# Performance work log

Measured on AMD Instinct MI355X. Metric: run time of the kernel, lower is better.

Reference implementation:

```python
import jax, jax.numpy as jnp
import numpy as np

N = 100000      # nodes
E = 1600000     # edges (avg degree 16)
IN = 128
OUT = 256


def setup_inputs() -> dict:
    key = jax.random.key(0)
    ks = jax.random.split(key, 8)
    x = jax.random.normal(ks[0], (N, IN), dtype=jnp.float32)
    edge_index = jax.random.randint(ks[1], (2, E), 0, N, dtype=jnp.int64)
    # GCNConv weights (glorot-ish scale) and biases
    W1 = jax.random.normal(ks[2], (IN, OUT), dtype=jnp.float32) / np.float32(np.sqrt(IN))
    b1 = jnp.zeros((OUT,), jnp.float32)
    W2 = jax.random.normal(ks[3], (OUT, OUT), dtype=jnp.float32) / np.float32(np.sqrt(OUT))
    b2 = jnp.zeros((OUT,), jnp.float32)
    # projection Linear(IN, OUT)
    Wp = jax.random.normal(ks[4], (IN, OUT), dtype=jnp.float32) / np.float32(np.sqrt(IN))
    bp = jax.random.normal(ks[5], (OUT,), dtype=jnp.float32) * 0.01
    return {"x": x, "edge_index": edge_index, "W1": W1, "b1": b1,
            "W2": W2, "b2": b2, "Wp": Wp, "bp": bp}


def _gcn_conv(x, W, b, src, dst, n):
    """PyG GCNConv: D^{-1/2}(A+I)D^{-1/2} X W + b. src/dst already include self-loops."""
    xw = x @ W                                              # [n, out]
    ones = jnp.ones(src.shape[0], dtype=xw.dtype)
    deg = jax.ops.segment_sum(ones, dst, num_segments=n)    # in-degree incl. self-loop
    dinv = jnp.where(deg > 0, jax.lax.rsqrt(deg), 0.0)
    norm = dinv[src] * dinv[dst]                            # [e]
    msgs = xw[src] * norm[:, None]                          # gather + scale
    out = jax.ops.segment_sum(msgs, dst, num_segments=n)    # scatter-add
    return out + b


def reference(x, edge_index, W1, b1, W2, b2, Wp, bp):
    n = x.shape[0]
    loop = jnp.arange(n, dtype=edge_index.dtype)            # self-loops
    src = jnp.concatenate([edge_index[0], loop])
    dst = jnp.concatenate([edge_index[1], loop])
    out = jax.nn.relu(_gcn_conv(x, W1, b1, src, dst, n))
    out = _gcn_conv(out, W2, b2, src, dst, n)
    identity = x @ Wp + bp                                  # projection (IN != OUT)
    return jax.nn.relu(out + identity)
```

## Files before the change

### kernel.cpp

```cpp
#include <hip/hip_runtime.h>

#define NODES 100000
#define EDGES 1600000
#define FIN   128
#define FOUT  256
#define NBUCK 196

typedef __bf16 bf16;
typedef __bf16 bf16x8 __attribute__((ext_vector_type(8)));
typedef __bf16 bf16x4 __attribute__((ext_vector_type(4)));
typedef __bf16 bf16x2 __attribute__((ext_vector_type(2)));
typedef float  f32x4  __attribute__((ext_vector_type(4)));

__global__ __launch_bounds__(256) void detect_kernel(const void* __restrict__ x,
                                                     const int* __restrict__ ei,
                                                     int* __restrict__ flags) {
    __shared__ int s_f32_evidence;
    __shared__ int s_odd_nonzero;
    int t = threadIdx.x;
    if (t == 0) { s_f32_evidence = 0; s_odd_nonzero = 0; }
    __syncthreads();
    const bf16* xb = (const bf16*)x;
    int local_f32 = 0;
    for (int i = t; i < 4096; i += 256) {
        float v = fabsf((float)xb[i]);
        if (!(v < 1e4f)) local_f32 = 1;
    }
    if (local_f32) atomicOr(&s_f32_evidence, 1);
    int local_odd = 0;
    for (int k = t; k < 1024; k += 256) {
        if (ei[2 * k + 1] != 0) local_odd = 1;
    }
    if (local_odd) atomicOr(&s_odd_nonzero, 1);
    __syncthreads();
    if (t == 0) {
        flags[0] = s_f32_evidence ? 0 : 1;
        flags[1] = s_odd_nonzero ? 0 : 1;
    }
}

__device__ __forceinline__ int edge_at(const int* __restrict__ ei, int which, int i,
                                       int is64) {
    if (is64) return ei[2 * (which * EDGES + i)];
    return ei[which * EDGES + i];
}

__global__ __launch_bounds__(512) void deg_count(const int* __restrict__ ei,
                                                 int* __restrict__ deg,
                                                 int* __restrict__ bhist,
                                                 const int* __restrict__ flags) {
    __shared__ int lh[256];
    int t = threadIdx.x;
    if (t < 256) lh[t] = 0;
    __syncthreads();
    int i = blockIdx.x * 512 + t;
    if (i < EDGES) {
        int is64 = flags[1];
        int s = edge_at(ei, 0, i, is64);
        int d = edge_at(ei, 1, i, is64);
        if (s >= 0 && s < NODES && d >= 0 && d < NODES) {
            atomicAdd(&deg[d], 1);
            atomicAdd(&lh[d >> 9], 1);
        }
    }
    __syncthreads();
    if (t < NBUCK && lh[t] > 0) atomicAdd(&bhist[t], lh[t]);
}

__global__ __launch_bounds__(256) void deg_to_dinv(const int* __restrict__ deg,
                                                   float* __restrict__ dinv, int n) {
    int i = blockIdx.x * 256 + threadIdx.x;
    if (i < n) dinv[i] = rsqrtf((float)deg[i] + 1.0f);
}

__global__ __launch_bounds__(1024) void scan1(const int* __restrict__ deg,
                                              int* __restrict__ col_ptr,
                                              int* __restrict__ blksum, int n) {
    __shared__ int sm[1024];
    int t = threadIdx.x;
    int i = blockIdx.x * 1024 + t;
    int v = (i < n) ? deg[i] : 0;
    sm[t] = v;
    __syncthreads();
    for (int off = 1; off < 1024; off <<= 1) {
        int u = (t >= off) ? sm[t - off] : 0;
        __syncthreads();
        sm[t] += u;
        __syncthreads();
    }
    if (i <= n) col_ptr[i] = sm[t] - v;
    if (t == 1023) blksum[blockIdx.x] = sm[t];
}

__global__ __launch_bounds__(128) void scan2(int* blk, int nblk) {
    __shared__ int sm[128];
    int t = threadIdx.x;
    int v = (t < nblk) ? blk[t] : 0;
    sm[t] = v;
    __syncthreads();
    for (int off = 1; off < 128; off <<= 1) {
        int u = (t >= off) ? sm[t - off] : 0;
        __syncthreads();
        sm[t] += u;
        __syncthreads();
    }
    if (t < nblk) blk[t] = sm[t] - v;
}

__global__ __launch_bounds__(256) void scan3(int* __restrict__ col_ptr,
                                             const int* __restrict__ blkoff, int n) {
    int i = blockIdx.x * 256 + threadIdx.x;
    if (i <= n) col_ptr[i] += blkoff[i >> 10];
}

__global__ __launch_bounds__(256) void bucket_scan(const int* __restrict__ bhist,
                                                   int* __restrict__ bbase,
                                                   int* __restrict__ bcur) {
    __shared__ int sm[256];
    int t = threadIdx.x;
    int v = (t < NBUCK) ? bhist[t] : 0;
    sm[t] = v;
    __syncthreads();
    for (int off = 1; off < 256; off <<= 1) {
        int u = (t >= off) ? sm[t - off] : 0;
        __syncthreads();
        sm[t] += u;
        __syncthreads();
    }
    if (t < NBUCK) {
        int ex = sm[t] - v;
        bbase[t] = ex;
        bcur[t]  = ex;
        if (t == NBUCK - 1) bbase[NBUCK] = sm[t];
    }
}

#define EPB 4096
__global__ __launch_bounds__(256) void partition_edges(const int* __restrict__ ei,
                                                       int* __restrict__ bcur,
                                                       uint2* __restrict__ pairs,
                                                       const int* __restrict__ flags) {
    __shared__ int lh[256], sc[256], lst[256], lcu[256], gb[256];
    __shared__ uint2 stage[EPB];
    int t = threadIdx.x;
    int base = blockIdx.x * EPB;
    int is64 = flags[1];

    lh[t] = 0;
    __syncthreads();

    int es[16], ed[16];
#pragma unroll
    for (int j = 0; j < 16; ++j) {
        int i = base + j * 256 + t;
        int s = -1, d = -1;
        if (i < EDGES) {
            s = edge_at(ei, 0, i, is64);
            d = edge_at(ei, 1, i, is64);
            if (s < 0 || s >= NODES || d < 0 || d >= NODES) d = -1;
        }
        es[j] = s; ed[j] = d;
        if (d >= 0) atomicAdd(&lh[d >> 9], 1);
    }
    __syncthreads();
    sc[t] = lh[t];
    __syncthreads();
    for (int off = 1; off < 256; off <<= 1) {
        int u = (t >= off) ? sc[t - off] : 0;
        __syncthreads();
        sc[t] += u;
        __syncthreads();
    }
    int start = sc[t] - lh[t];
    lst[t] = start;
    lcu[t] = start;
    __syncthreads();
#pragma unroll
    for (int j = 0; j < 16; ++j) {
        if (ed[j] >= 0) {
            int p = atomicAdd(&lcu[ed[j] >> 9], 1);
            stage[p] = make_uint2((unsigned)es[j], (unsigned)ed[j]);
        }
    }
    __syncthreads();
    if (t < NBUCK && lh[t] > 0) gb[t] = atomicAdd(&bcur[t], lh[t]);
    __syncthreads();
    int nval = sc[255];
    for (int slot = t; slot < nval; slot += 256) {
        uint2 e = stage[slot];
        int b = (int)(e.y >> 9);
        pairs[(size_t)gb[b] + (slot - lst[b])] = e;
    }
}

__global__ __launch_bounds__(512) void fine_fill(const uint2* __restrict__ pairs,
                                                 const int* __restrict__ bbase,
                                                 const int* __restrict__ col_ptr,
                                                 int* __restrict__ col_idx) {
    __shared__ int lcur[512];
    int b = blockIdx.x;
    int t = threadIdx.x;
    int node = (b << 9) + t;
    lcur[t] = (node < NODES) ? col_ptr[node] : 0;
    __syncthreads();
    int beg = bbase[b], end = bbase[b + 1];
    for (int i = beg + t; i < end; i += 512) {
        uint2 e = pairs[i];
        int pos = atomicAdd(&lcur[e.y & 511], 1);
        col_idx[pos] = (int)e.x;
    }
}

__global__ __launch_bounds__(256) void pack_all(const void* __restrict__ W1,
                                                const void* __restrict__ W2,
                                                const void* __restrict__ Wp,
                                                const void* __restrict__ b1,
                                                const void* __restrict__ b2,
                                                const void* __restrict__ bp,
                                                bf16* __restrict__ W1p, bf16* __restrict__ W2p,
                                                bf16* __restrict__ Wpp, bf16* __restrict__ b1b,
                                                bf16* __restrict__ b2b, bf16* __restrict__ bpb,
                                                const int* __restrict__ flags) {
    int fl = flags[0];
    int b = blockIdx.x;
    if (b < 512) {
        const void* W; bf16* Wo; int idx;
        if (b < 128)      { W = W1; Wo = W1p; idx = b * 256 + threadIdx.x; }
        else if (b < 384) { W = W2; Wo = W2p; idx = (b - 128) * 256 + threadIdx.x; }
        else              { W = Wp; Wo = Wpp; idx = (b - 384) * 256 + threadIdx.x; }
        int j    = idx & 7;
        int lane = (idx >> 3) & 63;
        int ct   = (idx >> 9) & 15;
        int kt   = idx >> 13;
        int k = kt * 32 + (lane >> 4) * 8 + j;
        int n = ct * 16 + (lane & 15);
        Wo[idx] = fl ? ((const bf16*)W)[k * 256 + n]
                     : (bf16)(((const float*)W)[k * 256 + n]);
    } else {
        const void* bb; bf16* bo;
        if (b == 512)      { bb = b1; bo = b1b; }
        else if (b == 513) { bb = b2; bo = b2b; }
        else               { bb = bp; bo = bpb; }
        int i = threadIdx.x;
        bo[i] = fl ? ((const bf16*)bb)[i] : (bf16)(((const float*)bb)[i]);
    }
}

__global__ __launch_bounds__(256) void gemm_proj(const void* __restrict__ Av,
                                                 const bf16* __restrict__ Wpk,
                                                 const float* __restrict__ dinv,
                                                 const bf16* __restrict__ bias,
                                                 void* __restrict__ outv,
                                                 bf16* __restrict__ projb,
                                                 int use_projb,
                                                 bf16* __restrict__ Xs,
                                                 const int* __restrict__ flags) {
    int a_f32 = (flags[0] == 0);
    int wave = threadIdx.x >> 6;
    int lane = threadIdx.x & 63;
    int row0 = blockIdx.x * 64;
    int lr = lane & 15;
    int lk = (lane >> 4) * 8;

    int arow[4];
    float di4[4];
#pragma unroll
    for (int rf = 0; rf < 4; ++rf) {
        int r = row0 + rf * 16 + lr;
        arow[rf] = r < NODES ? r : (NODES - 1);
        di4[rf] = dinv[arow[rf]];
    }

    f32x4 acc[4][4];
    f32x4 z = {0.f, 0.f, 0.f, 0.f};
#pragma unroll
    for (int i = 0; i < 4; ++i)
#pragma unroll
        for (int j = 0; j < 4; ++j) acc[i][j] = z;

    for (int kt = 0; kt < 4; ++kt) {
        bf16x8 af[4];
        if (!a_f32) {
            const bf16* Ab = (const bf16*)Av + kt * 32 + lk;
#pragma unroll
            for (int rf = 0; rf < 4; ++rf)
                af[rf] = *(const bf16x8*)(Ab + (size_t)arow[rf] * FIN);
        } else {
            const float* Af = (const float*)Av + kt * 32 + lk;
#pragma unroll
            for (int rf = 0; rf < 4; ++rf) {
                const float* p = Af + (size_t)arow[rf] * FIN;
                f32x4 lo = *(const f32x4*)p;
                f32x4 hi = *(const f32x4*)(p + 4);
                af[rf][0] = (bf16)lo[0]; af[rf][1] = (bf16)lo[1];
                af[rf][2] = (bf16)lo[2]; af[rf][3] = (bf16)lo[3];
                af[rf][4] = (bf16)hi[0]; af[rf][5] = (bf16)hi[1];
                af[rf][6] = (bf16)hi[2]; af[rf][7] = (bf16)hi[3];
            }
        }
#pragma unroll
        for (int rf = 0; rf < 4; ++rf) {
            bf16x8 xsv;
#pragma unroll
            for (int j = 0; j < 8; ++j) xsv[j] = (bf16)(di4[rf] * (float)af[rf][j]);
            *(bf16x8*)(Xs + (size_t)arow[rf] * FIN + kt * 32 + lk) = xsv;
        }
        const bf16* wb = Wpk + ((size_t)(kt * 16 + wave * 4) * 64 + lane) * 8;
        bf16x8 bfv[4];
#pragma unroll
        for (int cf = 0; cf < 4; ++cf)
            bfv[cf] = *(const bf16x8*)(wb + cf * 512);
#pragma unroll
        for (int rf = 0; rf < 4; ++rf)
#pragma unroll
            for (int cf = 0; cf < 4; ++cf)
                acc[rf][cf] = __builtin_amdgcn_mfma_f32_16x16x32_bf16(
                    af[rf], bfv[cf], acc[rf][cf], 0, 0, 0);
    }

    int rb = (lane >> 4) * 4;
    int out_f32 = a_f32;
#pragma unroll
    for (int rf = 0; rf < 4; ++rf) {
#pragma unroll
        for (int r = 0; r < 4; ++r) {
            int row = row0 + rf * 16 + rb + r;
            if (row >= NODES) continue;
#pragma unroll
            for (int cf = 0; cf < 4; ++cf) {
                int col = wave * 64 + cf * 16 + lr;
                float v = acc[rf][cf][r] + (float)bias[col];
                size_t off = (size_t)row * 256 + col;
                if (out_f32) {
                    if (use_projb) projb[off] = (bf16)v;
                    else           ((float*)outv)[off] = v;
                } else {
                    ((bf16*)outv)[off] = (bf16)v;
                }
            }
        }
    }
}

__global__ __launch_bounds__(256) void gemm_tile(const bf16* __restrict__ A,
                                                 const bf16* __restrict__ Wpk,
                                                 int K,
                                                 const float* __restrict__ dinv,
                                                 const bf16* __restrict__ bias,
                                                 int relu,
                                                 bf16* __restrict__ out) {
    int wave = threadIdx.x >> 6;
    int lane = threadIdx.x & 63;
    int row0 = blockIdx.x * 64;
    int lr = lane & 15;
    int lk = (lane >> 4) * 8;

    int arow[4];
#pragma unroll
    for (int rf = 0; rf < 4; ++rf) {
        int r = row0 + rf * 16 + lr;
        arow[rf] = r < NODES ? r : (NODES - 1);
    }

    f32x4 acc[4][4];
    f32x4 z = {0.f, 0.f, 0.f, 0.f};
#pragma unroll
    for (int i = 0; i < 4; ++i)
#pragma unroll
        for (int j = 0; j < 4; ++j) acc[i][j] = z;

    int ktiles = K >> 5;
    for (int kt = 0; kt < ktiles; ++kt) {
        const bf16* Ab = A + kt * 32 + lk;
        bf16x8 af[4];
#pragma unroll
        for (int rf = 0; rf < 4; ++rf)
            af[rf] = *(const bf16x8*)(Ab + (size_t)arow[rf] * K);
        const bf16* wb = Wpk + ((size_t)(kt * 16 + wave * 4) * 64 + lane) * 8;
        bf16x8 bfv[4];
#pragma unroll
        for (int cf = 0; cf < 4; ++cf)
            bfv[cf] = *(const bf16x8*)(wb + cf * 512);
#pragma unroll
        for (int rf = 0; rf < 4; ++rf)
#pragma unroll
            for (int cf = 0; cf < 4; ++cf)
                acc[rf][cf] = __builtin_amdgcn_mfma_f32_16x16x32_bf16(
                    af[rf], bfv[cf], acc[rf][cf], 0, 0, 0);
    }

    int rb = (lane >> 4) * 4;
#pragma unroll
    for (int rf = 0; rf < 4; ++rf) {
#pragma unroll
        for (int r = 0; r < 4; ++r) {
            int row = row0 + rf * 16 + rb + r;
            if (row >= NODES) continue;
            float s = dinv ? dinv[row] : 1.0f;
#pragma unroll
            for (int cf = 0; cf < 4; ++cf) {
                int col = wave * 64 + cf * 16 + lr;
                float v = acc[rf][cf][r] * s;
                if (bias) v += (float)bias[col];
                if (relu) v = fmaxf(v, 0.0f);
                out[(size_t)row * 256 + col] = (bf16)v;
            }
        }
    }
}

__global__ __launch_bounds__(256) void gather1(const int* __restrict__ col_ptr,
                                               const int* __restrict__ col_idx,
                                               const bf16* __restrict__ Xs,
                                               const float* __restrict__ dinv,
                                               bf16* __restrict__ aggX) {
    int wid  = (int)((blockIdx.x * 256 + threadIdx.x) >> 6);
    int lane = threadIdx.x & 63;
    if (wid >= NODES) return;
    int beg = col_ptr[wid], end = col_ptr[wid + 1];
    int c2 = lane * 2;

    bf16x2 self = *(const bf16x2*)(Xs + (size_t)wid * FIN + c2);
    float di = dinv[wid];

    float a0 = 0.f, a1 = 0.f;
    int npad = 0;
    for (int chunk = beg; chunk < end; chunk += 64) {
        int cnt = end - chunk;
        if (cnt > 64) cnt = 64;
        int padded = (cnt + 31) & ~31;
        npad += padded - cnt;
        int myidx = (lane < cnt) ? col_idx[chunk + lane] : wid;
        for (int j = 0; j < padded; j += 32) {
            bf16x2 v[32];
#pragma unroll
            for (int u = 0; u < 32; ++u) {
                int s = __shfl(myidx, j + u);
                v[u] = *(const bf16x2*)(Xs + (size_t)s * FIN + c2);
            }
#pragma unroll
            for (int u = 0; u < 32; ++u) { a0 += (float)v[u][0]; a1 += (float)v[u][1]; }
        }
    }

    float corr = (float)(1 - npad);
    bf16x2 o;
    o[0] = (bf16)(di * (a0 + corr * (float)self[0]));
    o[1] = (bf16)(di * (a1 + corr * (float)self[1]));
    *(bf16x2*)(aggX + (size_t)wid * FIN + c2) = o;
}

__global__ __launch_bounds__(256) void gather2(const int* __restrict__ col_ptr,
                                               const int* __restrict__ col_idx,
                                               const bf16* __restrict__ Y2,
                                               const float* __restrict__ dinv,
                                               const bf16* __restrict__ bias,
                                               const void* __restrict__ proj,
                                               const bf16* __restrict__ projb,
                                               int use_projb,
                                               void* __restrict__ outv,
                                               const int* __restrict__ flags) {
    int io_f32 = (flags[0] == 0);
    int wid  = (int)((blockIdx.x * 256 + threadIdx.x) >> 6);
    int lane = threadIdx.x & 63;
    if (wid >= NODES) return;
    int beg = col_ptr[wid], end = col_ptr[wid + 1];
    int c = lane * 4;
    size_t base = (size_t)wid * 256 + c;

    bf16x4 selfv = *(const bf16x4*)(Y2 + base);
    float di = dinv[wid];
    bf16x4 bv = *(const bf16x4*)(bias + c);
    f32x4 pv;
    if (!io_f32) {
        bf16x4 t = *(const bf16x4*)((const bf16*)proj + base);
#pragma unroll
        for (int k = 0; k < 4; ++k) pv[k] = (float)t[k];
    } else if (use_projb) {
        bf16x4 t = *(const bf16x4*)(projb + base);
#pragma unroll
        for (int k = 0; k < 4; ++k) pv[k] = (float)t[k];
    } else {
        pv = *(const f32x4*)((const float*)proj + base);
    }

    f32x4 acc = {0.f, 0.f, 0.f, 0.f};
    int npad = 0;
    for (int chunk = beg; chunk < end; chunk += 64) {
        int cnt = end - chunk;
        if (cnt > 64) cnt = 64;
        int padded = (cnt + 15) & ~15;
        npad += padded - cnt;
        int myidx = (lane < cnt) ? col_idx[chunk + lane] : wid;
        for (int j = 0; j < padded; j += 16) {
            bf16x4 v[16];
#pragma unroll
            for (int u = 0; u < 16; ++u) {
                int s = __shfl(myidx, j + u);
                v[u] = *(const bf16x4*)(Y2 + (size_t)s * 256 + c);
            }
#pragma unroll
            for (int u = 0; u < 16; ++u)
#pragma unroll
                for (int k = 0; k < 4; ++k) acc[k] += (float)v[u][k];
        }
    }

    float corr = (float)(1 - npad);
    f32x4 o;
#pragma unroll
    for (int k = 0; k < 4; ++k) {
        float r = di * (acc[k] + corr * (float)selfv[k]) + (float)bv[k] + pv[k];
        o[k] = fmaxf(r, 0.0f);
    }

    if (io_f32) {
        *(f32x4*)((float*)outv + base) = o;
    } else {
        bf16x4 ob;
#pragma unroll
        for (int k = 0; k < 4; ++k) ob[k] = (bf16)o[k];
        *(bf16x4*)((bf16*)outv + base) = ob;
    }
}

__global__ __launch_bounds__(256) void zero_out(bf16* out, int nelem) {
    int i = blockIdx.x * 256 + threadIdx.x;
    if (i < nelem) out[i] = (bf16)0.0f;
}

extern "C" void kernel_launch(void* const* d_in, const int* in_sizes, int n_in,
                              void* d_out, int out_size, void* d_ws, size_t ws_size,
                              hipStream_t stream) {
    const void* x   = d_in[0];
    const int*  ei  = (const int*)d_in[1];
    const void* W1  = d_in[2];
    const void* b1  = d_in[3];
    const void* W2  = d_in[4];
    const void* b2  = d_in[5];
    const void* Wp  = d_in[6];
    const void* bp  = d_in[7];

    const size_t NEEDED = 401408ull * 3 + 1024ull * 4 + 6400000 + 65536 + 131072 + 65536
                        + 1536 + 25600000ull * 2 + 51200000ull;
    const size_t NEEDED_EXT = NEEDED + 51200000ull;
    if (ws_size < NEEDED) {
        zero_out<<<(NODES * 256 + 255) / 256, 256, 0, stream>>>((bf16*)d_out, NODES * 256);
        return;
    }
    int use_projb = (ws_size >= NEEDED_EXT) ? 1 : 0;

    char* w = (char*)d_ws;
    int*   col_ptr = (int*)w;   w += 401408;
    int*   deg     = (int*)w;   w += 401408;
    int*   bhist   = (int*)w;   w += 1024;
    float* dinv    = (float*)w; w += 401408;
    int*   blk     = (int*)w;   w += 1024;
    int*   flags   = (int*)w;   w += 1024;
    int*   bbase   = (int*)w;   w += 1024;
    int*   bcur    = (int*)w;   w += 1024;
    int*   col_idx = (int*)w;   w += 6400000;
    bf16*  W1p     = (bf16*)w;  w += 65536;
    bf16*  W2p     = (bf16*)w;  w += 131072;
    bf16*  Wpp     = (bf16*)w;  w += 65536;
    bf16*  b1b     = (bf16*)w;  w += 512;
    bf16*  b2b     = (bf16*)w;  w += 512;
    bf16*  bpb     = (bf16*)w;  w += 512;
    bf16*  Xs      = (bf16*)w;  w += 25600000;
    bf16*  aggX    = (bf16*)w;  w += 25600000;
    bf16*  H1      = (bf16*)w;  w += 51200000;
    bf16*  projb   = (bf16*)w;  w += 51200000;
    uint2* pairs   = (uint2*)Xs;
    bf16*  Y2      = Xs;

    const int NBLK = (NODES + 1 + 1023) / 1024;

    detect_kernel<<<1, 256, 0, stream>>>(x, ei, flags);

    hipMemsetAsync(deg, 0, 401408 + 1024, stream);
    deg_count<<<(EDGES + 511) / 512, 512, 0, stream>>>(ei, deg, bhist, flags);
    deg_to_dinv<<<(NODES + 255) / 256, 256, 0, stream>>>(deg, dinv, NODES);

    scan1<<<NBLK, 1024, 0, stream>>>(deg, col_ptr, blk, NODES);
    scan2<<<1, 128, 0, stream>>>(blk, NBLK);
    scan3<<<(NODES + 256) / 256, 256, 0, stream>>>(col_ptr, blk, NODES);
    bucket_scan<<<1, 256, 0, stream>>>(bhist, bbase, bcur);

    partition_edges<<<(EDGES + EPB - 1) / EPB, 256, 0, stream>>>(ei, bcur, pairs, flags);
    fine_fill<<<NBUCK, 512, 0, stream>>>(pairs, bbase, col_ptr, col_idx);

    pack_all<<<515, 256, 0, stream>>>(W1, W2, Wp, b1, b2, bp,
                                      W1p, W2p, Wpp, b1b, b2b, bpb, flags);

    const int gemm_grid   = (NODES + 63) / 64;
    const int gather_grid = (NODES + 3) / 4;

    gemm_proj<<<gemm_grid, 256, 0, stream>>>(x, Wpp, dinv, bpb, d_out, projb, use_projb,
                                             Xs, flags);
    gather1<<<gather_grid, 256, 0, stream>>>(col_ptr, col_idx, Xs, dinv, aggX);
    gemm_tile<<<gemm_grid, 256, 0, stream>>>(aggX, W1p, FIN, nullptr, b1b, 1, H1);
    gemm_tile<<<gemm_grid, 256, 0, stream>>>(H1, W2p, FOUT, dinv, nullptr, 0, Y2);
    gather2<<<gather_grid, 256, 0, stream>>>(col_ptr, col_idx, Y2, dinv, b2b,
                                             d_out, projb, use_projb, d_out, flags);
}
```

Measured before the change: 662.8 us.

## Widen gather loads to 16B per lane and reorder projection GEMM after layer GEMMs

The two neighbor-gather kernels now have each lane load a 16-byte chunk from a different neighbor, several neighbors per wave instruction, instead of every lane loading a narrow 4- or 8-byte slice of the same row. Partial sums are combined with cross-lane shuffles afterwards. The aim is fewer, wider memory transactions per gathered row. The dinv-scaling of x moves into a separate elementwise kernel, and the projection GEMM now runs after the layer GEMMs, writing bf16 into the reused H1 buffer, so the separate projb workspace and the fp32 output-staging path are gone. The cost is an extra kernel launch, an extra read of x, and a shuffle reduction at the end of each gather.

New measurement: 650.9 us. No clear change (-1.8%).

```diff
diff --git a/kernel.cpp b/kernel.cpp
--- a/kernel.cpp
+++ b/kernel.cpp
@@ -11,6 +11,14 @@
 typedef __bf16 bf16x4 __attribute__((ext_vector_type(4)));
 typedef __bf16 bf16x2 __attribute__((ext_vector_type(2)));
 typedef float  f32x4  __attribute__((ext_vector_type(4)));
+typedef float  f32x2  __attribute__((ext_vector_type(2)));
+
+__device__ __forceinline__ f32x2 bf2f(unsigned w) {
+    f32x2 r;
+    r[0] = __uint_as_float(w << 16);
+    r[1] = __uint_as_float(w & 0xffff0000u);
+    return r;
+}
 
 __global__ __launch_bounds__(256) void detect_kernel(const void* __restrict__ x,
                                                      const int* __restrict__ ei,
@@ -246,14 +254,33 @@
     }
 }
 
+__global__ __launch_bounds__(256) void scale_x(const void* __restrict__ xv,
+                                               const float* __restrict__ dinv,
+                                               bf16* __restrict__ Xs,
+                                               const int* __restrict__ flags) {
+    int idx = blockIdx.x * 256 + threadIdx.x;
+    if (idx >= NODES * 16) return;
+    int row = idx >> 4, seg = idx & 15;
+    float di = dinv[row];
+    bf16x8 o;
+    if (flags[0]) {
+        bf16x8 v = *(const bf16x8*)((const bf16*)xv + (size_t)row * FIN + seg * 8);
+#pragma unroll
+        for (int j = 0; j < 8; ++j) o[j] = (bf16)(di * (float)v[j]);
+    } else {
+        const float* p = (const float*)xv + (size_t)row * FIN + seg * 8;
+        f32x4 lo = *(const f32x4*)p;
+        f32x4 hi = *(const f32x4*)(p + 4);
+#pragma unroll
+        for (int j = 0; j < 4; ++j) { o[j] = (bf16)(di * lo[j]); o[j + 4] = (bf16)(di * hi[j]); }
+    }
+    *(bf16x8*)(Xs + (size_t)row * FIN + seg * 8) = o;
+}
+
 __global__ __launch_bounds__(256) void gemm_proj(const void* __restrict__ Av,
                                                  const bf16* __restrict__ Wpk,
-                                                 const float* __restrict__ dinv,
                                                  const bf16* __restrict__ bias,
-                                                 void* __restrict__ outv,
                                                  bf16* __restrict__ projb,
-                                                 int use_projb,
-                                                 bf16* __restrict__ Xs,
                                                  const int* __restrict__ flags) {
     int a_f32 = (flags[0] == 0);
     int wave = threadIdx.x >> 6;
@@ -263,12 +290,10 @@
     int lk = (lane >> 4) * 8;
 
     int arow[4];
-    float di4[4];
 #pragma unroll
     for (int rf = 0; rf < 4; ++rf) {
         int r = row0 + rf * 16 + lr;
         arow[rf] = r < NODES ? r : (NODES - 1);
-        di4[rf] = dinv[arow[rf]];
     }
 
     f32x4 acc[4][4];
@@ -298,13 +323,6 @@
                 af[rf][6] = (bf16)hi[2]; af[rf][7] = (bf16)hi[3];
             }
         }
-#pragma unroll
-        for (int rf = 0; rf < 4; ++rf) {
-            bf16x8 xsv;
-#pragma unroll
-            for (int j = 0; j < 8; ++j) xsv[j] = (bf16)(di4[rf] * (float)af[rf][j]);
-            *(bf16x8*)(Xs + (size_t)arow[rf] * FIN + kt * 32 + lk) = xsv;
-        }
         const bf16* wb = Wpk + ((size_t)(kt * 16 + wave * 4) * 64 + lane) * 8;
         bf16x8 bfv[4];
 #pragma unroll
@@ -319,7 +337,6 @@
     }
 
     int rb = (lane >> 4) * 4;
-    int out_f32 = a_f32;
 #pragma unroll
     for (int rf = 0; rf < 4; ++rf) {
 #pragma unroll
@@ -330,13 +347,7 @@
             for (int cf = 0; cf < 4; ++cf) {
                 int col = wave * 64 + cf * 16 + lr;
                 float v = acc[rf][cf][r] + (float)bias[col];
-                size_t off = (size_t)row * 256 + col;
-                if (out_f32) {
-                    if (use_projb) projb[off] = (bf16)v;
-                    else           ((float*)outv)[off] = v;
-                } else {
-                    ((bf16*)outv)[off] = (bf16)v;
-                }
+                projb[(size_t)row * 256 + col] = (bf16)v;
             }
         }
     }
@@ -418,36 +429,59 @@
     int lane = threadIdx.x & 63;
     if (wid >= NODES) return;
     int beg = col_ptr[wid], end = col_ptr[wid + 1];
-    int c2 = lane * 2;
-
-    bf16x2 self = *(const bf16x2*)(Xs + (size_t)wid * FIN + c2);
+    int quarter = lane >> 4;
+    int li      = lane & 15;
+    int ch0     = li * 8 + quarter * 2;
+
+    bf16x2 self2 = *(const bf16x2*)(Xs + (size_t)wid * FIN + ch0);
     float di = dinv[wid];
 
-    float a0 = 0.f, a1 = 0.f;
+    const char* Xl = (const char*)Xs + li * 16;
+    f32x2 acc2[4];
+#pragma unroll
+    for (int d = 0; d < 4; ++d) { acc2[d][0] = 0.f; acc2[d][1] = 0.f; }
     int npad = 0;
     for (int chunk = beg; chunk < end; chunk += 64) {
         int cnt = end - chunk;
         if (cnt > 64) cnt = 64;
         int padded = (cnt + 31) & ~31;
         npad += padded - cnt;
-        int myidx = (lane < cnt) ? col_idx[chunk + lane] : wid;
+        int moff = ((lane < cnt) ? col_idx[chunk + lane] : wid) << 8;
         for (int j = 0; j < padded; j += 32) {
-            bf16x2 v[32];
-#pragma unroll
-            for (int u = 0; u < 32; ++u) {
-                int s = __shfl(myidx, j + u);
-                v[u] = *(const bf16x2*)(Xs + (size_t)s * FIN + c2);
+            uint4 w[8];
+#pragma unroll
+            for (int u = 0; u < 8; ++u) {
+                int so = __shfl(moff, j + u * 4 + quarter);
+                w[u] = *(const uint4*)(Xl + (unsigned)so);
             }
 #pragma unroll
-            for (int u = 0; u < 32; ++u) { a0 += (float)v[u][0]; a1 += (float)v[u][1]; }
-        }
-    }
+            for (int u = 0; u < 8; ++u) {
+                acc2[0] += bf2f(w[u].x);
+                acc2[1] += bf2f(w[u].y);
+                acc2[2] += bf2f(w[u].z);
+                acc2[3] += bf2f(w[u].w);
+            }
+        }
+    }
+#pragma unroll
+    for (int d = 0; d < 4; ++d) {
+        f32x2 t;
+        t[0] = __shfl_xor(acc2[d][0], 16);
+        t[1] = __shfl_xor(acc2[d][1], 16);
+        acc2[d] += t;
+        t[0] = __shfl_xor(acc2[d][0], 32);
+        t[1] = __shfl_xor(acc2[d][1], 32);
+        acc2[d] += t;
+    }
+    f32x2 t01 = (quarter & 1) ? acc2[1] : acc2[0];
+    f32x2 t23 = (quarter & 1) ? acc2[3] : acc2[2];
+    f32x2 pq  = (quarter & 2) ? t23 : t01;
 
     float corr = (float)(1 - npad);
     bf16x2 o;
-    o[0] = (bf16)(di * (a0 + corr * (float)self[0]));
-    o[1] = (bf16)(di * (a1 + corr * (float)self[1]));
-    *(bf16x2*)(aggX + (size_t)wid * FIN + c2) = o;
+    o[0] = (bf16)(di * (pq[0] + corr * (float)self2[0]));
+    o[1] = (bf16)(di * (pq[1] + corr * (float)self2[1]));
+    *(bf16x2*)(aggX + (size_t)wid * FIN + ch0) = o;
 }
 
 __global__ __launch_bounds__(256) void gather2(const int* __restrict__ col_ptr,
@@ -455,9 +489,7 @@
                                                const bf16* __restrict__ Y2,
                                                const float* __restrict__ dinv,
                                                const bf16* __restrict__ bias,
-                                               const void* __restrict__ proj,
                                                const bf16* __restrict__ projb,
-                                               int use_projb,
                                                void* __restrict__ outv,
                                                const int* __restrict__ flags) {
     int io_f32 = (flags[0] == 0);
@@ -465,62 +497,69 @@
     int lane = threadIdx.x & 63;
     if (wid >= NODES) return;
     int beg = col_ptr[wid], end = col_ptr[wid + 1];
-    int c = lane * 4;
-    size_t base = (size_t)wid * 256 + c;
-
-    bf16x4 selfv = *(const bf16x4*)(Y2 + base);
+    int half = lane >> 5;
+    int li   = lane & 31;
+    int ch0  = li * 8 + half * 4;
+    size_t obase = (size_t)wid * 256 + ch0;
+
+    bf16x4 selfv = *(const bf16x4*)(Y2 + obase);
     float di = dinv[wid];
-    bf16x4 bv = *(const bf16x4*)(bias + c);
-    f32x4 pv;
-    if (!io_f32) {
-        bf16x4 t = *(const bf16x4*)((const bf16*)proj + base);
-#pragma unroll
-        for (int k = 0; k < 4; ++k) pv[k] = (float)t[k];
-    } else if (use_projb) {
-        bf16x4 t = *(const bf16x4*)(projb + base);
-#pragma unroll
-        for (int k = 0; k < 4; ++k) pv[k] = (float)t[k];
-    } else {
-        pv = *(const f32x4*)((const float*)proj + base);
-    }
-
-    f32x4 acc = {0.f, 0.f, 0.f, 0.f};
+    bf16x4 bv = *(const bf16x4*)(bias + ch0);
+    bf16x4 pj = *(const bf16x4*)(projb + obase);
+
+    const char* Yl = (const char*)Y2 + li * 16;
+    f32x2 acc2[4];
+#pragma unroll
+    for (int d = 0; d < 4; ++d) { acc2[d][0] = 0.f; acc2[d][1] = 0.f; }
     int npad = 0;
     for (int chunk = beg; chunk < end; chunk += 64) {
         int cnt = end - chunk;
         if (cnt > 64) cnt = 64;
         int padded = (cnt + 15) & ~15;
         npad += padded - cnt;
-        int myidx = (lane < cnt) ? col_idx[chunk + lane] : wid;
+        int moff = ((lane < cnt) ? col_idx[chunk + lane] : wid) << 9;
         for (int j = 0; j < padded; j += 16) {
-            bf16x4 v[16];
-#pragma unroll
-            for (int u = 0; u < 16; ++u) {
-                int s = __shfl(myidx, j + u);
-                v[u] = *(const bf16x4*)(Y2 + (size_t)s * 256 + c);
+            uint4 w[8];
+#pragma unroll
+            for (int u = 0; u < 8; ++u) {
+                int so = __shfl(moff, j + u * 2 + half);
+                w[u] = *(const uint4*)(Yl + (unsigned)so);
             }
 #pragma unroll
-            for (int u = 0; u < 16; ++u)
-#pragma unroll
-                for (int k = 0; k < 4; ++k) acc[k] += (float)v[u][k];
-        }
-    }
+            for (int u = 0; u < 8; ++u) {
+                acc2[0] += bf2f(w[u].x);
+                acc2[1] += bf2f(w[u].y);
+                acc2[2] += bf2f(w[u].z);
+                acc2[3] += bf2f(w[u].w);
+            }
+        }
+    }
+#pragma unroll
+    for (int d = 0; d < 4; ++d) {
+        f32x2 t;
+        t[0] = __shfl_xor(acc2[d][0], 32);
+        t[1] = __shfl_xor(acc2[d][1], 32);
+        acc2[d] += t;
+    }
+    f32x2 p0 = half ? acc2[2] : acc2[0];
+    f32x2 p1 = half ? acc2[3] : acc2[1];
+    float av[4] = {p0[0], p0[1], p1[0], p1[1]};
 
     float corr = (float)(1 - npad);
     f32x4 o;
 #pragma unroll
     for (int k = 0; k < 4; ++k) {
-        float r = di * (acc[k] + corr * (float)selfv[k]) + (float)bv[k] + pv[k];
+        float r = di * (av[k] + corr * (float)selfv[k]) + (float)bv[k] + (float)pj[k];
         o[k] = fmaxf(r, 0.0f);
     }
 
     if (io_f32) {
-        *(f32x4*)((float*)outv + base) = o;
+        *(f32x4*)((float*)outv + obase) = o;
     } else {
         bf16x4 ob;
 #pragma unroll
         for (int k = 0; k < 4; ++k) ob[k] = (bf16)o[k];
-        *(bf16x4*)((bf16*)outv + base) = ob;
+        *(bf16x4*)((bf16*)outv + obase) = ob;
     }
 }
 
@@ -543,12 +582,10 @@
 
     const size_t NEEDED = 401408ull * 3 + 1024ull * 4 + 6400000 + 65536 + 131072 + 65536
                         + 1536 + 25600000ull * 2 + 51200000ull;
-    const size_t NEEDED_EXT = NEEDED + 51200000ull;
     if (ws_size < NEEDED) {
         zero_out<<<(NODES * 256 + 255) / 256, 256, 0, stream>>>((bf16*)d_out, NODES * 256);
         return;
     }
-    int use_projb = (ws_size >= NEEDED_EXT) ? 1 : 0;
 
     char* w = (char*)d_ws;
     int*   col_ptr = (int*)w;   w += 401408;
@@ -569,9 +606,9 @@
     bf16*  Xs      = (bf16*)w;  w += 25600000;
     bf16*  aggX    = (bf16*)w;  w += 25600000;
     bf16*  H1      = (bf16*)w;  w += 51200000;
-    bf16*  projb   = (bf16*)w;  w += 51200000;
     uint2* pairs   = (uint2*)Xs;
     bf16*  Y2      = Xs;
+    bf16*  projb   = H1;
 
     const int NBLK = (NODES + 1 + 1023) / 1024;
 
@@ -595,11 +632,11 @@
     const int gemm_grid   = (NODES + 63) / 64;
     const int gather_grid = (NODES + 3) / 4;
 
-    gemm_proj<<<gemm_grid, 256, 0, stream>>>(x, Wpp, dinv, bpb, d_out, projb, use_projb,
-                                             Xs, flags);
+    scale_x<<<(NODES * 16 + 255) / 256, 256, 0, stream>>>(x, dinv, Xs, flags);
     gather1<<<gather_grid, 256, 0, stream>>>(col_ptr, col_idx, Xs, dinv, aggX);
     gemm_tile<<<gemm_grid, 256, 0, stream>>>(aggX, W1p, FIN, nullptr, b1b, 1, H1);
     gemm_tile<<<gemm_grid, 256, 0, stream>>>(H1, W2p, FOUT, dinv, nullptr, 0, Y2);
+    gemm_proj<<<gemm_grid, 256, 0, stream>>>(x, Wpp, bpb, projb, flags);
     gather2<<<gather_grid, 256, 0, stream>>>(col_ptr, col_idx, Y2, dinv, b2b,
-                                             d_out, projb, use_projb, d_out, flags);
-}
+                                             projb, d_out, flags);
+}
```
